# Kernel optimization log

Measured on AMD Instinct MI355X. Metric: run time of the kernel, lower is better.

Reference implementation:

```python
import jax, jax.numpy as jnp
from jax import lax
import numpy as np

IMG = 2048.0            # square image size (W=H)
STRIDES = [32, 64, 128]
FEATS = [64, 32, 16]    # IMG / stride
NUM_CLASSES = 80
BATCH = 8
SCORE_THRESH = 0.2
NMS_THRESH = 0.6
TOPK = 1000             # topk_candidates per level
DETS = 100              # detections_per_img


def make_anchors(fs, stride):
    # square anchors of size==stride centered on the feature grid (AnchorGenerator with ratio 1.0)
    c = (jnp.arange(fs, dtype=jnp.float32) + 0.5) * stride
    cy, cx = jnp.meshgrid(c, c, indexing='ij')
    cx, cy = cx.reshape(-1), cy.reshape(-1)
    h = stride / 2.0
    return jnp.stack([cx - h, cy - h, cx + h, cy + h], axis=1)


def setup_inputs() -> dict:
    key = jax.random.key(0)
    inp = {}
    for i, (fs, s) in enumerate(zip(FEATS, STRIDES)):
        hw = fs * fs
        key, k1, k2, k3 = jax.random.split(key, 4)
        inp[f'cls{i}'] = jax.random.normal(k1, (BATCH, hw, NUM_CLASSES), jnp.float32)
        inp[f'reg{i}'] = jax.random.uniform(k2, (BATCH, hw, 4), jnp.float32)
        inp[f'ctr{i}'] = jax.random.normal(k3, (BATCH, hw), jnp.float32)
        inp[f'anc{i}'] = make_anchors(fs, float(s))
    return inp


def _decode(rel, boxes):
    # BoxLinearCoder.decode_single with normalize_by_size=True
    cx = 0.5 * (boxes[:, 0] + boxes[:, 2])
    cy = 0.5 * (boxes[:, 1] + boxes[:, 3])
    w = boxes[:, 2] - boxes[:, 0]
    h = boxes[:, 3] - boxes[:, 1]
    rel = rel * jnp.stack([w, h, w, h], axis=1)
    return jnp.stack([cx - rel[:, 0], cy - rel[:, 1], cx + rel[:, 2], cy + rel[:, 3]], axis=1)


def _iou(b):
    # torchvision box_iou on a single set of boxes [N,4] -> [N,N]
    area = (b[:, 2] - b[:, 0]) * (b[:, 3] - b[:, 1])
    lt = jnp.maximum(b[:, None, :2], b[None, :, :2])
    rb = jnp.minimum(b[:, None, 2:], b[None, :, 2:])
    wh = jnp.clip(rb - lt, 0.0)
    inter = wh[..., 0] * wh[..., 1]
    return inter / (area[:, None] + area[None, :] - inter)


def _greedy_keep(iou):
    # classic greedy NMS on score-sorted boxes: suppress j>i with iou>thresh if i kept
    n = iou.shape[0]
    idx = jnp.arange(n)
    def body(i, keep):
        supp = keep[i] & (iou[i] > NMS_THRESH) & (idx > i)
        return keep & ~supp
    return lax.fori_loop(0, n, body, jnp.ones((n,), bool))


def _per_image(cls_l, reg_l, ctr_l, anc_l):
    boxes, scores, labels = [], [], []
    for cls, reg, ctr, anc in zip(cls_l, reg_l, ctr_l, anc_l):
        hw, c = cls.shape
        # scores = sqrt(sigmoid(cls) * sigmoid(ctrness)) flattened over anchors*classes
        sc = jnp.sqrt(jax.nn.sigmoid(cls) * jax.nn.sigmoid(ctr)[:, None]).reshape(-1)
        sc = jnp.where(sc > SCORE_THRESH, sc, -1.0)  # score threshold as mask (static shapes)
        ts, ti = lax.top_k(sc, TOPK)                 # per-level top-k candidates
        aidx = ti // c
        lab = ti % c
        b = jnp.clip(_decode(reg[aidx], anc[aidx]), 0.0, IMG)  # decode + clip to image
        boxes.append(b); scores.append(ts); labels.append(lab)
    boxes = jnp.concatenate(boxes)    # [3*TOPK, 4]
    scores = jnp.concatenate(scores)  # [3*TOPK]
    labels = jnp.concatenate(labels)  # [3*TOPK]
    n = scores.shape[0]
    # batched_nms via per-class coordinate offsets
    off = labels.astype(boxes.dtype) * (IMG + 1.0)
    ss, oi = lax.top_k(scores, n)     # sort candidates by score desc
    bs = boxes[oi] + off[oi][:, None]
    keep = lax.stop_gradient(_greedy_keep(_iou(bs)))
    fsc = jnp.where(keep & (ss > 0), ss, -1.0)
    fs, fi = lax.top_k(fsc, DETS)     # keep detections_per_img; score==-1 marks padding
    return boxes[oi][fi], fs, labels[oi][fi]


def reference(cls0, cls1, cls2, reg0, reg1, reg2, ctr0, ctr1, ctr2, anc0, anc1, anc2):
    f = jax.vmap(lambda c0, c1, c2, r0, r1, r2, t0, t1, t2: _per_image(
        [c0, c1, c2], [r0, r1, r2], [t0, t1, t2], [anc0, anc1, anc2]))
    return f(cls0, cls1, cls2, reg0, reg1, reg2, ctr0, ctr1, ctr2)
```

## Files before the change

### kernel.cpp

```cpp
#include <hip/hip_runtime.h>

#define NCLS  80
#define SELK  512
#define NLVL  3
#define NIMG  8
#define DETS  100
#define CAP   1024
#define NSORT 4096
#define NDEC  1024
#define HBINS 4096
#define NHBLK 16
#define NCBLK 64
#define QBASE 0x3F800000u
#define QMAX  0x41C80000u
#define IMGSZ 2048.0f


__device__ __forceinline__ float sigm(float x) {
    if (x >= 0.f) return 1.f / (1.f + expf(-x));
    float e = expf(x);
    return e / (1.f + e);
}

__device__ __forceinline__ unsigned int qbits(float ea, float t1) {
    return __float_as_uint(__fmul_rn(__fadd_rn(1.f, ea), t1));
}

__device__ __forceinline__ void bitonic_desc(unsigned long long* s, int N) {
    for (int k = 2; k <= N; k <<= 1) {
        for (int j = k >> 1; j > 0; j >>= 1) {
            __syncthreads();
            for (int i = threadIdx.x; i < N; i += blockDim.x) {
                int ixj = i ^ j;
                if (ixj > i) {
                    unsigned long long a = s[i], b = s[ixj];
                    bool up = ((i & k) == 0);
                    if (up ? (a < b) : (a > b)) { s[i] = b; s[ixj] = a; }
                }
            }
        }
    }
    __syncthreads();
}

__device__ __forceinline__ void lvl_select(int level,
    const float* c0, const float* c1, const float* c2,
    const float* t0, const float* t1, const float* t2,
    const float** cls, const float** ctr, int* hw) {
    if (level == 0)      { *cls = c0; *ctr = t0; *hw = 4096; }
    else if (level == 1) { *cls = c1; *ctr = t1; *hw = 1024; }
    else                 { *cls = c2; *ctr = t2; *hw = 256; }
}


__global__ void k_hist(const float* c0, const float* c1, const float* c2,
                       const float* t0, const float* t1, const float* t2,
                       unsigned int* parts, unsigned int* counters) {
    int level = blockIdx.z, img = blockIdx.y;
    int pair = img * NLVL + level;
    if (blockIdx.x == 0 && threadIdx.x == 0) counters[pair * 16] = 0;
    const float* cls; const float* ctr; int hw;
    lvl_select(level, c0, c1, c2, t0, t1, t2, &cls, &ctr, &hw);
    int n4 = hw * (NCLS / 4);
    const float4* cl4 = (const float4*)(cls + (size_t)img * hw * NCLS);
    const float* ct = ctr + (size_t)img * hw;
    __shared__ unsigned int h[HBINS];
    for (int i = threadIdx.x; i < HBINS; i += 256) h[i] = 0;
    __syncthreads();
    for (int i = blockIdx.x * 256 + threadIdx.x; i < n4; i += NHBLK * 256) {
        float4 v = cl4[i];
        int a = i / (NCLS / 4);
        float eb = expf(-ct[a]);
        float t1 = __fadd_rn(1.f, eb);
        #pragma unroll
        for (int k = 0; k < 4; ++k) {
            float x = (k == 0) ? v.x : (k == 1) ? v.y : (k == 2) ? v.z : v.w;
            unsigned int qb = qbits(expf(-x), t1);
            if (qb < QMAX) {
                unsigned int bin = (qb - QBASE) >> 13;
                if (bin > HBINS - 1) bin = HBINS - 1;
                atomicAdd(&h[bin], 1u);
            }
        }
    }
    __syncthreads();
    unsigned int* P = parts + ((size_t)(pair * NHBLK + blockIdx.x)) * HBINS;
    for (int i = threadIdx.x; i < HBINS; i += 256) P[i] = h[i];
}


__global__ void k_find(const unsigned int* parts, unsigned int* vcut) {
    int pair = blockIdx.x;
    int tid = threadIdx.x;
    __shared__ unsigned int hb[HBINS];
    __shared__ unsigned int segsum[256];
    __shared__ unsigned int pref[256];
    unsigned int acc[HBINS / 256];
    #pragma unroll
    for (int j = 0; j < HBINS / 256; ++j) acc[j] = 0;
    for (int blk = 0; blk < NHBLK; ++blk) {
        const unsigned int* P = parts + ((size_t)(pair * NHBLK + blk)) * HBINS;
        #pragma unroll
        for (int j = 0; j < HBINS / 256; ++j) acc[j] += P[tid + 256 * j];
    }
    #pragma unroll
    for (int j = 0; j < HBINS / 256; ++j) hb[tid + 256 * j] = acc[j];
    __syncthreads();
    unsigned int seg = 0;
    #pragma unroll
    for (int j = 0; j < 16; ++j) seg += hb[16 * tid + j];
    segsum[tid] = seg;
    pref[tid] = seg;
    __syncthreads();
    for (int off = 1; off < 256; off <<= 1) {
        unsigned int v = (tid >= off) ? pref[tid - off] : 0u;
        __syncthreads();
        pref[tid] += v;
        __syncthreads();
    }
    unsigned int incl = pref[tid];
    unsigned int excl = incl - seg;
    if (excl < (unsigned int)SELK && incl >= (unsigned int)SELK) {
        unsigned int cum = excl; int B = HBINS - 1;
        for (int b = 16 * tid; b < 16 * tid + 16; ++b) {
            cum += hb[b];
            if (cum >= (unsigned int)SELK) { B = b; break; }
        }
        vcut[pair] = (B >= HBINS - 1) ? QMAX : (QBASE + ((unsigned int)(B + 1) << 13));
    }
    if (tid == 255 && pref[255] < (unsigned int)SELK)
        vcut[pair] = QMAX;
}


__global__ void k_collect(const float* c0, const float* c1, const float* c2,
                          const float* t0, const float* t1, const float* t2,
                          const unsigned int* vcut, unsigned int* counters,
                          unsigned long long* buf) {
    int level = blockIdx.z, img = blockIdx.y;
    const float* cls; const float* ctr; int hw;
    lvl_select(level, c0, c1, c2, t0, t1, t2, &cls, &ctr, &hw);
    int n4 = hw * (NCLS / 4);
    int pair = img * NLVL + level;
    const float4* cl4 = (const float4*)(cls + (size_t)img * hw * NCLS);
    const float* ct = ctr + (size_t)img * hw;
    unsigned int V = vcut[pair];
    __shared__ unsigned long long sbuf[CAP];
    __shared__ unsigned int scnt;
    __shared__ unsigned int sbase;
    if (threadIdx.x == 0) scnt = 0;
    __syncthreads();
    for (int i = blockIdx.x * 256 + threadIdx.x; i < n4; i += NCBLK * 256) {
        float4 v = cl4[i];
        int a = i / (NCLS / 4);
        float cta = ct[a];
        float eb = expf(-cta);
        float t1 = __fadd_rn(1.f, eb);
        #pragma unroll
        for (int k = 0; k < 4; ++k) {
            float x = (k == 0) ? v.x : (k == 1) ? v.y : (k == 2) ? v.z : v.w;
            unsigned int qb = qbits(expf(-x), t1);
            if (qb < V) {
                float s = sqrtf(sigm(x) * sigm(cta));
                unsigned int e = (unsigned int)(4 * i + k);
                unsigned int p = ((unsigned int)level << 19) | e;
                unsigned int slot = atomicAdd(&scnt, 1u);
                if (slot < CAP)
                    sbuf[slot] = ((unsigned long long)__float_as_uint(s) << 32) | (~p);
            }
        }
    }
    __syncthreads();
    unsigned int cl_n = scnt; if (cl_n > CAP) cl_n = CAP;
    if (threadIdx.x == 0)
        sbase = atomicAdd(&counters[pair * 16], cl_n);
    __syncthreads();
    unsigned int base = sbase;
    for (unsigned int idx = threadIdx.x; idx < cl_n; idx += 256) {
        unsigned int g = base + idx;
        if (g < CAP) buf[(size_t)pair * CAP + g] = sbuf[idx];
    }
}


__global__ void __launch_bounds__(1024)
k_merge_nms(const unsigned long long* buf, const unsigned int* counters,
            const float* r0, const float* r1, const float* r2,
            const float* a0, const float* a1, const float* a2,
            float* out) {
    int img = blockIdx.x;
    int tid = threadIdx.x;
    __shared__ unsigned long long S[NSORT];
    __shared__ float4 wbox[NDEC];
    __shared__ int    wlab[NDEC];
    __shared__ float4 sbx[64]; __shared__ float sar[64];
    __shared__ float4 koff[DETS]; __shared__ float karr[DETS];
    __shared__ float4 kb[DETS]; __shared__ float ks[DETS]; __shared__ int kl[DETS];
    __shared__ float4 rb[DETS]; __shared__ int rl[DETS];

    for (int l = 0; l < NLVL; ++l) {
        int pair = img * NLVL + l;
        int c = (int)counters[pair * 16]; if (c > CAP) c = CAP;
        const unsigned long long* B = buf + (size_t)pair * CAP;
        for (int i = tid; i < CAP; i += 1024)
            S[l * CAP + i] = (i < c) ? B[i] : 0ull;
    }
    for (int i = NLVL * CAP + tid; i < NSORT; i += 1024) S[i] = 0ull;
    bitonic_desc(S, NSORT);

    {
        unsigned long long key = S[tid];
        float4 b4 = make_float4(0.f, 0.f, 0.f, 0.f); int lbv = 0;
        if (key != 0ull) {
            unsigned int p = (~((unsigned int)key)) & 0x1FFFFFu;
            int lvl = (int)(p >> 19);
            unsigned int e = p & 0x7FFFFu;
            int a = (int)(e / NCLS); lbv = (int)(e % NCLS);
            const float* anc; const float* reg; int hw;
            if (lvl == 0)      { anc = a0; reg = r0; hw = 4096; }
            else if (lvl == 1) { anc = a1; reg = r1; hw = 1024; }
            else               { anc = a2; reg = r2; hw = 256; }
            const float* rg = reg + (size_t)img * hw * 4;
            float ax1 = anc[a * 4 + 0], ay1 = anc[a * 4 + 1];
            float ax2 = anc[a * 4 + 2], ay2 = anc[a * 4 + 3];
            float cx = 0.5f * (ax1 + ax2), cy = 0.5f * (ay1 + ay2);
            float w = ax2 - ax1, h = ay2 - ay1;
            float e0 = rg[a * 4 + 0] * w, e1 = rg[a * 4 + 1] * h;
            float e2 = rg[a * 4 + 2] * w, e3 = rg[a * 4 + 3] * h;
            b4.x = fminf(fmaxf(cx - e0, 0.f), IMGSZ);
            b4.y = fminf(fmaxf(cy - e1, 0.f), IMGSZ);
            b4.z = fminf(fmaxf(cx + e2, 0.f), IMGSZ);
            b4.w = fminf(fmaxf(cy + e3, 0.f), IMGSZ);
        }
        wbox[tid] = b4; wlab[tid] = lbv;
    }
    __syncthreads();

    if (tid >= 64) return;
    int lane = tid;
    unsigned long long lmask_lt = (lane == 0) ? 0ull : (~0ull >> (64 - lane));

    int kept = 0, ring = 0, r = 0;

    while (kept < DETS && r < NDEC) {
        int rank = r + lane;
        unsigned long long key = (rank < NDEC) ? S[rank] : 0ull;
        unsigned int bits = (unsigned int)(key >> 32);
        unsigned long long pm = __ballot(bits != 0u);
        int npos = (pm == ~0ull) ? 64 : (int)__builtin_ctzll(~pm);
        if (npos == 0) break;

        float4 bx = make_float4(0.f, 0.f, 0.f, 0.f); int lb = 0;
        if (lane < npos) { bx = wbox[rank]; lb = wlab[rank]; }
        float off = (float)lb * (IMGSZ + 1.0f);
        float ox1 = bx.x + off, oy1 = bx.y + off;
        float ox2 = bx.z + off, oy2 = bx.w + off;
        float car = (ox2 - ox1) * (oy2 - oy1);
        sbx[lane] = make_float4(ox1, oy1, ox2, oy2);
        sar[lane] = car;

        bool supk = false;
        for (int k2 = 0; k2 < kept; ++k2) {
            float4 kk = koff[k2]; float ka = karr[k2];
            float lx = fmaxf(kk.x, ox1), ly = fmaxf(kk.y, oy1);
            float rx = fminf(kk.z, ox2), ry = fminf(kk.w, oy2);
            float w = fmaxf(rx - lx, 0.f), h = fmaxf(ry - ly, 0.f);
            float inter = w * h;
            supk = supk || (inter / (ka + car - inter) > 0.6f);
        }
        unsigned long long col = 0ull;
        for (int i = 0; i < npos; ++i) {
            float4 c = sbx[i]; float ca = sar[i];
            float lx = fmaxf(c.x, ox1), ly = fmaxf(c.y, oy1);
            float rx = fminf(c.z, ox2), ry = fminf(c.w, oy2);
            float w = fmaxf(rx - lx, 0.f), h = fmaxf(ry - ly, 0.f);
            float inter = w * h;
            if ((inter / (ca + car - inter) > 0.6f) && (i < lane)) col |= (1ull << i);
        }
        unsigned long long undecided = __ballot((lane < npos) && !supk);
        unsigned long long aliveSel = 0ull;
        int capleft = DETS - kept;
        int lastSlot = npos - 1;
        while (undecided) {
            int i = (int)__builtin_ctzll(undecided);
            aliveSel |= (1ull << i);
            undecided &= ~(1ull << i);
            if (--capleft == 0) { lastSlot = i; break; }
            unsigned long long row = __ballot(((col >> i) & 1ull) != 0ull);
            undecided &= ~row;
        }
        unsigned long long region = (lastSlot >= 63) ? ~0ull : ((1ull << (lastSlot + 1)) - 1ull);
        region &= (npos >= 64) ? ~0ull : ((1ull << npos) - 1ull);
        unsigned long long rejm = region & ~aliveSel;

        if ((aliveSel >> lane) & 1ull) {
            int ki = kept + (int)__popcll(aliveSel & lmask_lt);
            koff[ki] = make_float4(ox1, oy1, ox2, oy2); karr[ki] = car;
            kb[ki] = bx; ks[ki] = __uint_as_float(bits); kl[ki] = lb;
        }
        if ((rejm >> lane) & 1ull) {
            int ri = ring + (int)__popcll(rejm & lmask_lt);
            if (ri < DETS) { rb[ri] = bx; rl[ri] = lb; }
        }
        kept += (int)__popcll(aliveSel);
        ring += (int)__popcll(rejm);
        r += lastSlot + 1;
    }

    while (kept < DETS && ring < DETS && r < NDEC) {
        int rank = r + lane;
        if (rank < NDEC) {
            int ri = ring + lane;
            if (ri < DETS) { rb[ri] = wbox[rank]; rl[ri] = wlab[rank]; }
        }
        int take = NDEC - r; if (take > 64) take = 64;
        ring += take;
        r += 64;
    }

    for (int k = lane; k < DETS; k += 64) {
        float4 bxo; float scv; int lv;
        if (k < kept) { bxo = kb[k]; scv = ks[k]; lv = kl[k]; }
        else { int q = k - kept; bxo = rb[q]; scv = -1.0f; lv = rl[q]; }
        float* ob = out + ((size_t)img * DETS + k) * 4;
        ob[0] = bxo.x; ob[1] = bxo.y; ob[2] = bxo.z; ob[3] = bxo.w;
        out[NIMG * DETS * 4 + img * DETS + k] = scv;
        out[NIMG * DETS * 5 + img * DETS + k] = (float)lv;
    }
}


extern "C" void kernel_launch(void* const* d_in, const int* in_sizes, int n_in,
                              void* d_out, int out_size, void* d_ws, size_t ws_size,
                              hipStream_t stream) {
    (void)in_sizes; (void)n_in; (void)out_size; (void)ws_size;
    const float* cls0 = (const float*)d_in[0];
    const float* reg0 = (const float*)d_in[1];
    const float* ctr0 = (const float*)d_in[2];
    const float* anc0 = (const float*)d_in[3];
    const float* cls1 = (const float*)d_in[4];
    const float* reg1 = (const float*)d_in[5];
    const float* ctr1 = (const float*)d_in[6];
    const float* anc1 = (const float*)d_in[7];
    const float* cls2 = (const float*)d_in[8];
    const float* reg2 = (const float*)d_in[9];
    const float* ctr2 = (const float*)d_in[10];
    const float* anc2 = (const float*)d_in[11];
    float* out = (float*)d_out;
    char* ws = (char*)d_ws;

    const size_t OFF_PARTS = 0;
    const size_t OFF_CNT   = 6291456;
    const size_t OFF_VCUT  = 6292992;
    const size_t OFF_BUF   = 6293120;

    unsigned int* parts = (unsigned int*)(ws + OFF_PARTS);
    unsigned int* cnt   = (unsigned int*)(ws + OFF_CNT);
    unsigned int* vcut  = (unsigned int*)(ws + OFF_VCUT);
    unsigned long long* buf  = (unsigned long long*)(ws + OFF_BUF);

    k_hist<<<dim3(NHBLK, NIMG, NLVL), 256, 0, stream>>>(
        cls0, cls1, cls2, ctr0, ctr1, ctr2, parts, cnt);
    k_find<<<24, 256, 0, stream>>>(parts, vcut);
    k_collect<<<dim3(NCBLK, NIMG, NLVL), 256, 0, stream>>>(
        cls0, cls1, cls2, ctr0, ctr1, ctr2, vcut, cnt, buf);
    k_merge_nms<<<NIMG, 1024, 0, stream>>>(buf, cnt, reg0, reg1, reg2,
                                           anc0, anc1, anc2, out);
}
```

Baseline: 195.3 us.

## Fuse threshold search into collect and replace 4096 bitonic sort with merge

```diff
diff --git a/kernel.cpp b/kernel.cpp
--- a/kernel.cpp
+++ b/kernel.cpp
@@ -6,11 +6,10 @@
 #define NIMG  8
 #define DETS  100
 #define CAP   1024
-#define NSORT 4096
 #define NDEC  1024
 #define HBINS 4096
 #define NHBLK 16
-#define NCBLK 64
+#define NCBLK 16
 #define QBASE 0x3F800000u
 #define QMAX  0x41C80000u
 #define IMGSZ 2048.0f
@@ -24,23 +23,6 @@
 
 __device__ __forceinline__ unsigned int qbits(float ea, float t1) {
     return __float_as_uint(__fmul_rn(__fadd_rn(1.f, ea), t1));
-}
-
-__device__ __forceinline__ void bitonic_desc(unsigned long long* s, int N) {
-    for (int k = 2; k <= N; k <<= 1) {
-        for (int j = k >> 1; j > 0; j >>= 1) {
-            __syncthreads();
-            for (int i = threadIdx.x; i < N; i += blockDim.x) {
-                int ixj = i ^ j;
-                if (ixj > i) {
-                    unsigned long long a = s[i], b = s[ixj];
-                    bool up = ((i & k) == 0);
-                    if (up ? (a < b) : (a > b)) { s[i] = b; s[ixj] = a; }
-                }
-            }
-        }
-    }
-    __syncthreads();
 }
 
 __device__ __forceinline__ void lvl_select(int level,
@@ -89,68 +71,67 @@
 }
 
 
-__global__ void k_find(const unsigned int* parts, unsigned int* vcut) {
-    int pair = blockIdx.x;
+__global__ void k_collect(const float* c0, const float* c1, const float* c2,
+                          const float* t0, const float* t1, const float* t2,
+                          const unsigned int* parts, unsigned int* counters,
+                          unsigned long long* buf) {
+    int level = blockIdx.z, img = blockIdx.y;
+    int pair = img * NLVL + level;
     int tid = threadIdx.x;
     __shared__ unsigned int hb[HBINS];
     __shared__ unsigned int segsum[256];
     __shared__ unsigned int pref[256];
-    unsigned int acc[HBINS / 256];
-    #pragma unroll
-    for (int j = 0; j < HBINS / 256; ++j) acc[j] = 0;
-    for (int blk = 0; blk < NHBLK; ++blk) {
-        const unsigned int* P = parts + ((size_t)(pair * NHBLK + blk)) * HBINS;
-        #pragma unroll
-        for (int j = 0; j < HBINS / 256; ++j) acc[j] += P[tid + 256 * j];
-    }
-    #pragma unroll
-    for (int j = 0; j < HBINS / 256; ++j) hb[tid + 256 * j] = acc[j];
-    __syncthreads();
-    unsigned int seg = 0;
-    #pragma unroll
-    for (int j = 0; j < 16; ++j) seg += hb[16 * tid + j];
-    segsum[tid] = seg;
-    pref[tid] = seg;
-    __syncthreads();
-    for (int off = 1; off < 256; off <<= 1) {
-        unsigned int v = (tid >= off) ? pref[tid - off] : 0u;
+    __shared__ unsigned long long sbuf[CAP];
+    __shared__ unsigned int scnt, sbase, Vsh;
+    if (tid == 0) scnt = 0;
+    {
+        unsigned int acc[HBINS / 256];
+        #pragma unroll
+        for (int j = 0; j < HBINS / 256; ++j) acc[j] = 0;
+        for (int blk = 0; blk < NHBLK; ++blk) {
+            const unsigned int* P = parts + ((size_t)(pair * NHBLK + blk)) * HBINS;
+            #pragma unroll
+            for (int j = 0; j < HBINS / 256; ++j) acc[j] += P[tid + 256 * j];
+        }
+        #pragma unroll
+        for (int j = 0; j < HBINS / 256; ++j) hb[tid + 256 * j] = acc[j];
+    }
+    __syncthreads();
+    {
+        unsigned int seg = 0;
+        #pragma unroll
+        for (int j = 0; j < 16; ++j) seg += hb[16 * tid + j];
+        segsum[tid] = seg;
+        pref[tid] = seg;
         __syncthreads();
-        pref[tid] += v;
-        __syncthreads();
-    }
-    unsigned int incl = pref[tid];
-    unsigned int excl = incl - seg;
-    if (excl < (unsigned int)SELK && incl >= (unsigned int)SELK) {
-        unsigned int cum = excl; int B = HBINS - 1;
-        for (int b = 16 * tid; b < 16 * tid + 16; ++b) {
-            cum += hb[b];
-            if (cum >= (unsigned int)SELK) { B = b; break; }
-        }
-        vcut[pair] = (B >= HBINS - 1) ? QMAX : (QBASE + ((unsigned int)(B + 1) << 13));
-    }
-    if (tid == 255 && pref[255] < (unsigned int)SELK)
-        vcut[pair] = QMAX;
-}
-
-
-__global__ void k_collect(const float* c0, const float* c1, const float* c2,
-                          const float* t0, const float* t1, const float* t2,
-                          const unsigned int* vcut, unsigned int* counters,
-                          unsigned long long* buf) {
-    int level = blockIdx.z, img = blockIdx.y;
+        for (int off = 1; off < 256; off <<= 1) {
+            unsigned int v = (tid >= off) ? pref[tid - off] : 0u;
+            __syncthreads();
+            pref[tid] += v;
+            __syncthreads();
+        }
+        unsigned int incl = pref[tid];
+        unsigned int excl = incl - segsum[tid];
+        if (excl < (unsigned int)SELK && incl >= (unsigned int)SELK) {
+            unsigned int cum = excl; int B = HBINS - 1;
+            for (int b = 16 * tid; b < 16 * tid + 16; ++b) {
+                cum += hb[b];
+                if (cum >= (unsigned int)SELK) { B = b; break; }
+            }
+            Vsh = (B >= HBINS - 1) ? QMAX : (QBASE + ((unsigned int)(B + 1) << 13));
+        }
+        if (tid == 255 && pref[255] < (unsigned int)SELK)
+            Vsh = QMAX;
+    }
+    __syncthreads();
+    unsigned int V = Vsh;
+
     const float* cls; const float* ctr; int hw;
     lvl_select(level, c0, c1, c2, t0, t1, t2, &cls, &ctr, &hw);
     int n4 = hw * (NCLS / 4);
-    int pair = img * NLVL + level;
     const float4* cl4 = (const float4*)(cls + (size_t)img * hw * NCLS);
     const float* ct = ctr + (size_t)img * hw;
-    unsigned int V = vcut[pair];
-    __shared__ unsigned long long sbuf[CAP];
-    __shared__ unsigned int scnt;
-    __shared__ unsigned int sbase;
-    if (threadIdx.x == 0) scnt = 0;
-    __syncthreads();
-    for (int i = blockIdx.x * 256 + threadIdx.x; i < n4; i += NCBLK * 256) {
+    for (int i = blockIdx.x * 256 + tid; i < n4; i += NCBLK * 256) {
         float4 v = cl4[i];
         int a = i / (NCLS / 4);
         float cta = ct[a];
@@ -172,11 +153,11 @@
     }
     __syncthreads();
     unsigned int cl_n = scnt; if (cl_n > CAP) cl_n = CAP;
-    if (threadIdx.x == 0)
+    if (tid == 0)
         sbase = atomicAdd(&counters[pair * 16], cl_n);
     __syncthreads();
     unsigned int base = sbase;
-    for (unsigned int idx = threadIdx.x; idx < cl_n; idx += 256) {
+    for (unsigned int idx = tid; idx < cl_n; idx += 256) {
         unsigned int g = base + idx;
         if (g < CAP) buf[(size_t)pair * CAP + g] = sbuf[idx];
     }
@@ -190,24 +171,65 @@
             float* out) {
     int img = blockIdx.x;
     int tid = threadIdx.x;
-    __shared__ unsigned long long S[NSORT];
-    __shared__ float4 wbox[NDEC];
-    __shared__ int    wlab[NDEC];
+    __shared__ unsigned long long S[3 * CAP];
+    __shared__ unsigned long long Mbuf[2 * CAP];
     __shared__ float4 sbx[64]; __shared__ float sar[64];
     __shared__ float4 koff[DETS]; __shared__ float karr[DETS];
     __shared__ float4 kb[DETS]; __shared__ float ks[DETS]; __shared__ int kl[DETS];
     __shared__ float4 rb[DETS]; __shared__ int rl[DETS];
+    float4* wbox = (float4*)Mbuf;
+    int*    wlab = (int*)(S + CAP);
 
     for (int l = 0; l < NLVL; ++l) {
         int pair = img * NLVL + l;
         int c = (int)counters[pair * 16]; if (c > CAP) c = CAP;
         const unsigned long long* B = buf + (size_t)pair * CAP;
-        for (int i = tid; i < CAP; i += 1024)
-            S[l * CAP + i] = (i < c) ? B[i] : 0ull;
-    }
-    for (int i = NLVL * CAP + tid; i < NSORT; i += 1024) S[i] = 0ull;
-    bitonic_desc(S, NSORT);
-
+        S[l * CAP + tid] = (tid < c) ? B[tid] : 0ull;
+    }
+    for (int k2 = 2; k2 <= CAP; k2 <<= 1) {
+        for (int j = k2 >> 1; j > 0; j >>= 1) {
+            __syncthreads();
+            int i = tid;
+            int ixj = i ^ j;
+            if (ixj > i) {
+                bool up = ((i & k2) == 0);
+                #pragma unroll
+                for (int seg = 0; seg < NLVL; ++seg) {
+                    int base = seg * CAP;
+                    unsigned long long a = S[base + i], b = S[base + ixj];
+                    if (up ? (a < b) : (a > b)) { S[base + i] = b; S[base + ixj] = a; }
+                }
+            }
+        }
+    }
+    __syncthreads();
+    for (int k = tid; k < 2 * CAP; k += 1024) {
+        int lo = max(0, k - CAP), hi = min(k, CAP);
+        while (lo < hi) {
+            int mid = (lo + hi) >> 1;
+            if (S[mid] > S[CAP + (k - mid - 1)]) lo = mid + 1; else hi = mid;
+        }
+        int i = lo, j = k - lo;
+        unsigned long long av = (i < CAP) ? S[i] : 0ull;
+        unsigned long long bv = (j < CAP) ? S[CAP + j] : 0ull;
+        Mbuf[k] = (av > bv) ? av : bv;
+    }
+    __syncthreads();
+    {
+        int k = tid;
+        int lo = max(0, k - CAP), hi = k;
+        while (lo < hi) {
+            int mid = (lo + hi) >> 1;
+            if (Mbuf[mid] > S[2 * CAP + (k - mid - 1)]) lo = mid + 1; else hi = mid;
+        }
+        int i = lo, j = k - lo;
+        unsigned long long mv = (i < 2 * CAP) ? Mbuf[i] : 0ull;
+        unsigned long long cv = (j < CAP) ? S[2 * CAP + j] : 0ull;
+        unsigned long long rk = (mv > cv) ? mv : cv;
+        __syncthreads();
+        S[k] = rk;
+    }
+    __syncthreads();
     {
         unsigned long long key = S[tid];
         float4 b4 = make_float4(0.f, 0.f, 0.f, 0.f); int lbv = 0;
@@ -351,19 +373,16 @@
 
     const size_t OFF_PARTS = 0;
     const size_t OFF_CNT   = 6291456;
-    const size_t OFF_VCUT  = 6292992;
-    const size_t OFF_BUF   = 6293120;
+    const size_t OFF_BUF   = 6292992;
 
     unsigned int* parts = (unsigned int*)(ws + OFF_PARTS);
     unsigned int* cnt   = (unsigned int*)(ws + OFF_CNT);
-    unsigned int* vcut  = (unsigned int*)(ws + OFF_VCUT);
-    unsigned long long* buf  = (unsigned long long*)(ws + OFF_BUF);
+    unsigned long long* buf = (unsigned long long*)(ws + OFF_BUF);
 
     k_hist<<<dim3(NHBLK, NIMG, NLVL), 256, 0, stream>>>(
         cls0, cls1, cls2, ctr0, ctr1, ctr2, parts, cnt);
-    k_find<<<24, 256, 0, stream>>>(parts, vcut);
     k_collect<<<dim3(NCBLK, NIMG, NLVL), 256, 0, stream>>>(
-        cls0, cls1, cls2, ctr0, ctr1, ctr2, vcut, cnt, buf);
+        cls0, cls1, cls2, ctr0, ctr1, ctr2, parts, cnt, buf);
     k_merge_nms<<<NIMG, 1024, 0, stream>>>(buf, cnt, reg0, reg1, reg2,
                                            anc0, anc1, anc2, out);
 }
```

Result: faster. 177.6 us (-9.0%).
